# Performance work log

Hardware: AMD Instinct MI355X
Metric: run time of the kernel (lower is better)

## Reference

```python
import jax, jax.numpy as jnp
import numpy as np

N, D_IN, D_SAE, K = 8192, 768, 24576, 32


def setup_inputs() -> dict:
    key = jax.random.key(0)
    k1, k2, k3 = jax.random.split(key, 3)
    x = jax.random.normal(k1, (N, D_IN), dtype=jnp.float32)
    # kaiming_uniform_ on empty(d_in, d_sae): bound = sqrt(6 / d_in) (fan_in = d_sae? torch uses
    # fan_in = size(1) = d_sae for W_enc; we just need a same-scale random init for a reference)
    b_enc_bound = np.sqrt(6.0 / D_SAE)
    W_enc = jax.random.uniform(k2, (D_IN, D_SAE), dtype=jnp.float32,
                               minval=-b_enc_bound, maxval=b_enc_bound)
    b_dec_bound = np.sqrt(6.0 / D_IN)
    W_dec = jax.random.uniform(k3, (D_SAE, D_IN), dtype=jnp.float32,
                               minval=-b_dec_bound, maxval=b_dec_bound)
    # module normalizes decoder rows to unit L2 norm at init
    W_dec = W_dec / jnp.linalg.norm(W_dec, axis=1, keepdims=True)
    b_enc = jnp.zeros((D_SAE,), dtype=jnp.float32)
    b_dec = jnp.zeros((D_IN,), dtype=jnp.float32)
    return {"x": x, "W_enc": W_enc, "b_enc": b_enc, "W_dec": W_dec, "b_dec": b_dec}


def reference(x, W_enc, b_enc, W_dec, b_dec):
    # encode: relu((x - b_dec) @ W_enc + b_enc)
    z = jax.nn.relu((x - b_dec) @ W_enc + b_enc)            # [N, d_sae]
    topk_vals, topk_inds = jax.lax.top_k(z, K)              # [N, K]
    rows = jnp.arange(z.shape[0])[:, None]                  # [N, 1]
    z_sparse = jnp.zeros_like(z).at[rows, topk_inds].set(topk_vals)
    x_reconstruct = z_sparse @ W_dec + b_dec                # [N, d_in]
    return (x_reconstruct, z_sparse)
```

## Files before the change

kernel.cpp:

```cpp
#include <hip/hip_runtime.h>

#define N_ROWS 8192
#define D_IN   768
#define D_SAE  24576
#define K_TOP  32
#define C_SEL  40
#define DELTA  2e-4f

typedef __attribute__((ext_vector_type(8))) short bf16x8;
typedef __attribute__((ext_vector_type(4))) float f32x4;

__device__ __forceinline__ ushort f2bf(float f) {
    const unsigned u = __float_as_uint(f);
    return (ushort)((u + 0x7FFFu + ((u >> 16) & 1u)) >> 16);
}
__device__ __forceinline__ float bf2f(ushort h) {
    return __uint_as_float(((unsigned)h) << 16);
}

#define GBM 128
#define GBN 192
#define GBK 32

__global__ __launch_bounds__(256)
void sae_cvt_x(const float* __restrict__ x, const float* __restrict__ b_dec,
               ushort* __restrict__ ahi, ushort* __restrict__ alo)
{
    const int idx = blockIdx.x * 256 + threadIdx.x;
    const int i   = idx * 4;
    const int k   = (idx % (D_IN / 4)) * 4;
    const float4 xv = *(const float4*)(&x[i]);
    const float4 bd = *(const float4*)(&b_dec[k]);
    const float e[4] = {xv.x - bd.x, xv.y - bd.y, xv.z - bd.z, xv.w - bd.w};
    ushort h[4], l[4];
#pragma unroll
    for (int j = 0; j < 4; ++j) {
        h[j] = f2bf(e[j]);
        l[j] = f2bf(e[j] - bf2f(h[j]));
    }
    *(ushort4*)(&ahi[i]) = make_ushort4(h[0], h[1], h[2], h[3]);
    *(ushort4*)(&alo[i]) = make_ushort4(l[0], l[1], l[2], l[3]);
}

__global__ __launch_bounds__(256)
void sae_cvt_w(const float* __restrict__ W_enc,
               ushort* __restrict__ bhi, ushort* __restrict__ blo)
{
    __shared__ float tile[32][33];
    const int n0 = blockIdx.x * 32;
    const int k0 = blockIdx.y * 32;
    const int t  = threadIdx.x;
    const int r  = t >> 3;
    const int c4 = (t & 7) * 4;
    *(float4*)(&tile[r][c4]) = *(const float4*)(&W_enc[(size_t)(k0 + r) * D_SAE + n0 + c4]);
    __syncthreads();
    ushort h[4], l[4];
#pragma unroll
    for (int j = 0; j < 4; ++j) {
        const float e = tile[c4 + j][r];
        h[j] = f2bf(e);
        l[j] = f2bf(e - bf2f(h[j]));
    }
    *(ushort4*)(&bhi[(size_t)(n0 + r) * D_IN + k0 + c4]) = make_ushort4(h[0], h[1], h[2], h[3]);
    *(ushort4*)(&blo[(size_t)(n0 + r) * D_IN + k0 + c4]) = make_ushort4(l[0], l[1], l[2], l[3]);
}

__global__ __launch_bounds__(256, 2)
void sae_encode_mfma3(const ushort* __restrict__ ahi, const ushort* __restrict__ alo,
                      const ushort* __restrict__ bhi, const ushort* __restrict__ blo,
                      const float* __restrict__ b_enc, float* __restrict__ z)
{
    __shared__ ushort A_lds[2][2][4][GBM][8];
    __shared__ ushort B_lds[2][2][4][GBN][8];

    const int tid  = threadIdx.x;
    const int lane = tid & 63;
    const int wid  = tid >> 6;
    const int wr   = wid >> 1;
    const int wc   = wid & 1;
    const int l15  = lane & 15;
    const int lc   = lane >> 4;

    const int col0  = blockIdx.y * GBN;
    const int arow0 = blockIdx.x * GBM;
    const int row_w = arow0 + wr * 64;

    const int NT = D_IN / GBK;

    f32x4 acc[4][6];
#pragma unroll
    for (int i = 0; i < 4; ++i)
#pragma unroll
        for (int j = 0; j < 6; ++j) acc[i][j] = (f32x4){0.f, 0.f, 0.f, 0.f};

    bf16x8 s0, s1, s2, s3, s4, s5, s6, s7, s8, s9;

#define LOADQ(J, DST) { \
        const int q = (J) * 4 + wid; \
        if ((J) < 4) { \
            const int pl = q & 1, c = (q >> 1) & 3, h = q >> 3; \
            DST = *(const bf16x8*)((pl ? alo : ahi) + (size_t)(arow0 + h * 64 + lane) * D_IN + k0s + c * 8); \
        } else { \
            const int r2 = q - 16; \
            const int pl = r2 & 1, c = (r2 >> 1) & 3, g = r2 >> 3; \
            DST = *(const bf16x8*)((pl ? blo : bhi) + (size_t)(col0 + g * 64 + lane) * D_IN + k0s + c * 8); \
        } }

#define WRITEQ(J, SRC, BUF) { \
        const int q = (J) * 4 + wid; \
        if ((J) < 4) { \
            const int pl = q & 1, c = (q >> 1) & 3, h = q >> 3; \
            *(bf16x8*)(&A_lds[BUF][pl][c][h * 64 + lane][0]) = SRC; \
        } else { \
            const int r2 = q - 16; \
            const int pl = r2 & 1, c = (r2 >> 1) & 3, g = r2 >> 3; \
            *(bf16x8*)(&B_lds[BUF][pl][c][g * 64 + lane][0]) = SRC; \
        } }

#define LOAD_ALL() { LOADQ(0, s0) LOADQ(1, s1) LOADQ(2, s2) LOADQ(3, s3) LOADQ(4, s4) \
                     LOADQ(5, s5) LOADQ(6, s6) LOADQ(7, s7) LOADQ(8, s8) LOADQ(9, s9) }
#define WRITE_ALL(BUF) { WRITEQ(0, s0, BUF) WRITEQ(1, s1, BUF) WRITEQ(2, s2, BUF) WRITEQ(3, s3, BUF) \
                         WRITEQ(4, s4, BUF) WRITEQ(5, s5, BUF) WRITEQ(6, s6, BUF) WRITEQ(7, s7, BUF) \
                         WRITEQ(8, s8, BUF) WRITEQ(9, s9, BUF) }

    {
        const int k0s = 0;
        LOAD_ALL();
    }
    WRITE_ALL(0);
    __syncthreads();

    for (int kt = 0; kt < NT; ++kt) {
        const int cur = kt & 1;
        if (kt + 1 < NT) {
            const int k0s = (kt + 1) * GBK;
            LOAD_ALL();
        }

        bf16x8 bh[6], bl[6];
#pragma unroll
        for (int ct = 0; ct < 6; ++ct) {
            const int n = wc * 96 + ct * 16 + l15;
            bh[ct] = *(const bf16x8*)(&B_lds[cur][0][lc][n][0]);
            bl[ct] = *(const bf16x8*)(&B_lds[cur][1][lc][n][0]);
        }
#pragma unroll
        for (int rt = 0; rt < 4; ++rt) {
            const int m = wr * 64 + rt * 16 + l15;
            const bf16x8 ah = *(const bf16x8*)(&A_lds[cur][0][lc][m][0]);
            const bf16x8 al = *(const bf16x8*)(&A_lds[cur][1][lc][m][0]);
#pragma unroll
            for (int ct = 0; ct < 6; ++ct) {
                acc[rt][ct] = __builtin_amdgcn_mfma_f32_16x16x32_bf16(ah, bh[ct], acc[rt][ct], 0, 0, 0);
                acc[rt][ct] = __builtin_amdgcn_mfma_f32_16x16x32_bf16(ah, bl[ct], acc[rt][ct], 0, 0, 0);
                acc[rt][ct] = __builtin_amdgcn_mfma_f32_16x16x32_bf16(al, bh[ct], acc[rt][ct], 0, 0, 0);
            }
        }

        if (kt + 1 < NT) {
            WRITE_ALL(cur ^ 1);
            __syncthreads();
        }
    }

#undef LOAD_ALL
#undef WRITE_ALL
#undef LOADQ
#undef WRITEQ

#pragma unroll
    for (int ct = 0; ct < 6; ++ct) {
        const int col = col0 + wc * 96 + ct * 16 + l15;
        const float bec = b_enc[col];
#pragma unroll
        for (int rt = 0; rt < 4; ++rt) {
            const int rowb = row_w + rt * 16 + lc * 4;
#pragma unroll
            for (int r = 0; r < 4; ++r)
                z[(size_t)(rowb + r) * D_SAE + col] = fmaxf(acc[rt][ct][r] + bec, 0.f);
        }
    }
}

__global__ __launch_bounds__(256, 2)
void sae_encode_mfma(const float* __restrict__ x,
                     const float* __restrict__ W_enc,
                     const float* __restrict__ b_enc,
                     const float* __restrict__ b_dec,
                     float* __restrict__ z)
{
    __shared__ ushort Bs[2][4][GBN][8];

    const int tid  = threadIdx.x;
    const int lane = tid & 63;
    const int wid  = tid >> 6;
    const int wr   = wid >> 1;
    const int wc   = wid & 1;
    const int l15  = lane & 15;
    const int lc   = lane >> 4;

    const int col0  = blockIdx.x * GBN;
    const int row_w = blockIdx.y * GBM + wr * 64;

    f32x4 acc[4][6];
#pragma unroll
    for (int i = 0; i < 4; ++i)
#pragma unroll
        for (int j = 0; j < 6; ++j) acc[i][j] = (f32x4){0.f, 0.f, 0.f, 0.f};

    for (int kt = 0; kt < D_IN / GBK; ++kt) {
        const int k0 = kt * GBK;

        float bvv[3][8];
#pragma unroll
        for (int np = 0; np < 3; ++np)
#pragma unroll
            for (int it = 0; it < 8; ++it)
                bvv[np][it] = W_enc[(size_t)(k0 + wid * 8 + it) * D_SAE + col0 + np * 64 + lane];

        const float4 bd0 = *(const float4*)(&b_dec[k0 + lc * 8]);
        const float4 bd1 = *(const float4*)(&b_dec[k0 + lc * 8 + 4]);
        bf16x8 ah[4], al[4];
#pragma unroll
        for (int rt = 0; rt < 4; ++rt) {
            const size_t off = (size_t)(row_w + rt * 16 + l15) * D_IN + k0 + lc * 8;
            const float4 a0 = *(const float4*)(&x[off]);
            const float4 a1 = *(const float4*)(&x[off + 4]);
            float e[8];
            e[0] = a0.x - bd0.x; e[1] = a0.y - bd0.y; e[2] = a0.z - bd0.z; e[3] = a0.w - bd0.w;
            e[4] = a1.x - bd1.x; e[5] = a1.y - bd1.y; e[6] = a1.z - bd1.z; e[7] = a1.w - bd1.w;
#pragma unroll
            for (int j = 0; j < 8; ++j) {
                const ushort h = f2bf(e[j]);
                ah[rt][j] = (short)h;
                al[rt][j] = (short)f2bf(e[j] - bf2f(h));
            }
        }

        uint4 bh_pk[3], bl_pk[3];
#pragma unroll
        for (int np = 0; np < 3; ++np) {
            ushort h[8], l[8];
#pragma unroll
            for (int it = 0; it < 8; ++it) {
                h[it] = f2bf(bvv[np][it]);
                l[it] = f2bf(bvv[np][it] - bf2f(h[it]));
            }
            bh_pk[np] = make_uint4((unsigned)h[0] | ((unsigned)h[1] << 16),
                                   (unsigned)h[2] | ((unsigned)h[3] << 16),
                                   (unsigned)h[4] | ((unsigned)h[5] << 16),
                                   (unsigned)h[6] | ((unsigned)h[7] << 16));
            bl_pk[np] = make_uint4((unsigned)l[0] | ((unsigned)l[1] << 16),
                                   (unsigned)l[2] | ((unsigned)l[3] << 16),
                                   (unsigned)l[4] | ((unsigned)l[5] << 16),
                                   (unsigned)l[6] | ((unsigned)l[7] << 16));
        }

        __syncthreads();
#pragma unroll
        for (int np = 0; np < 3; ++np) {
            const int n = np * 64 + lane;
            *(uint4*)(&Bs[0][wid][n][0]) = bh_pk[np];
            *(uint4*)(&Bs[1][wid][n][0]) = bl_pk[np];
        }
        __syncthreads();

#pragma unroll
        for (int ct = 0; ct < 6; ++ct) {
            const int n = wc * 96 + ct * 16 + l15;
            const bf16x8 bh = *(const bf16x8*)(&Bs[0][lc][n][0]);
            const bf16x8 bl = *(const bf16x8*)(&Bs[1][lc][n][0]);
#pragma unroll
            for (int rt = 0; rt < 4; ++rt) {
                acc[rt][ct] = __builtin_amdgcn_mfma_f32_16x16x32_bf16(ah[rt], bh, acc[rt][ct], 0, 0, 0);
                acc[rt][ct] = __builtin_amdgcn_mfma_f32_16x16x32_bf16(ah[rt], bl, acc[rt][ct], 0, 0, 0);
                acc[rt][ct] = __builtin_amdgcn_mfma_f32_16x16x32_bf16(al[rt], bh, acc[rt][ct], 0, 0, 0);
            }
        }
    }

#pragma unroll
    for (int ct = 0; ct < 6; ++ct) {
        const int col = col0 + wc * 96 + ct * 16 + l15;
        const float bec = b_enc[col];
#pragma unroll
        for (int rt = 0; rt < 4; ++rt) {
            const int rowb = row_w + rt * 16 + lc * 4;
#pragma unroll
            for (int r = 0; r < 4; ++r)
                z[(size_t)(rowb + r) * D_SAE + col] = fmaxf(acc[rt][ct][r] + bec, 0.f);
        }
    }
}

#define TB     256
#define QPT    (D_SAE / 4 / TB)
#define HB     2048
#define NCOPY  2
#define BNDCAP 248
#define POOLN  288
#define NCAND  6
#define NEGF   -1e30f
#define BADIDX (1 << 30)

__global__ __launch_bounds__(TB, 4)
void sae_topk_decode(float* __restrict__ z,
                     const float* __restrict__ x,
                     const float* __restrict__ W_enc,
                     const float* __restrict__ b_enc,
                     const float* __restrict__ W_dec,
                     const float* __restrict__ b_dec,
                     float* __restrict__ x_rec)
{
    __shared__ int    hist[NCOPY * HB];
    __shared__ int    sufx[TB];
    __shared__ float  poolv[POOLN];
    __shared__ int    pooli[POOLN];
    __shared__ float  selv[C_SEL];
    __shared__ int    seli[C_SEL];
    __shared__ float  xrow[D_IN];
    __shared__ double cand[C_SEL];
    __shared__ int    shB, shChi;
    __shared__ int    nDef, nBnd, nFail;

    const int row = blockIdx.x;
    const int t   = threadIdx.x;
    const int w   = t >> 6;
    float* zr = z + (size_t)row * D_SAE;

    for (int i = t; i < NCOPY * HB; i += TB) hist[i] = 0;
    if (t == 0) { nDef = 0; nBnd = 0; nFail = 0; }
    __syncthreads();

    float cv[NCAND]; int ci[NCAND];
#pragma unroll
    for (int j = 0; j < NCAND; ++j) { cv[j] = NEGF; ci[j] = BADIDX; }
    {
        int* hw = &hist[(w >> 1) * HB];
        int zc = 0;
        for (int i0 = 0; i0 < QPT; i0 += 8) {
            f32x4 va[8];
#pragma unroll
            for (int u2 = 0; u2 < 8; ++u2)
                va[u2] = __builtin_nontemporal_load((const f32x4*)(&zr[(size_t)(t + (i0 + u2) * TB) * 4]));
#pragma unroll
            for (int u2 = 0; u2 < 8; ++u2) {
                const int base = (t + (i0 + u2) * TB) * 4;
#define PROC(f, o) { \
        const unsigned uu = __float_as_uint(f); \
        if (uu) atomicAdd(&hw[uu >> 20], 1); else ++zc; \
        const bool b0 = (f) > cv[0]; const bool b1 = (f) > cv[1]; const bool b2 = (f) > cv[2]; \
        const bool b3 = (f) > cv[3]; const bool b4 = (f) > cv[4]; const bool b5 = (f) > cv[5]; \
        if (b5) { \
            cv[5] = b4 ? cv[4] : (f);        ci[5] = b4 ? ci[4] : (base + o); \
            if (b4) { cv[4] = b3 ? cv[3] : (f); ci[4] = b3 ? ci[3] : (base + o); } \
            if (b3) { cv[3] = b2 ? cv[2] : (f); ci[3] = b2 ? ci[2] : (base + o); } \
            if (b2) { cv[2] = b1 ? cv[1] : (f); ci[2] = b1 ? ci[1] : (base + o); } \
            if (b1) { cv[1] = b0 ? cv[0] : (f); ci[1] = b0 ? ci[0] : (base + o); } \
            if (b0) { cv[0] = (f); ci[0] = (base + o); } \
        } }
                PROC(va[u2][0], 0) PROC(va[u2][1], 1) PROC(va[u2][2], 2) PROC(va[u2][3], 3)
#undef PROC
            }
        }
        if (zc) atomicAdd(&hw[0], zc);
    }
    __syncthreads();

    int cnt8[8]; int tot = 0;
#pragma unroll
    for (int j = 0; j < 8; ++j) {
        const int b = t * 8 + j;
        const int c = hist[b] + hist[HB + b];
        cnt8[j] = c; tot += c;
    }
    sufx[t] = tot;
    __syncthreads();
    for (int off = 1; off < TB; off <<= 1) {
        const int a = sufx[t];
        const int b = (t + off < TB) ? sufx[t + off] : 0;
        __syncthreads();
        sufx[t] = a + b;
        __syncthreads();
    }
    {
        int run = (t + 1 < TB) ? sufx[t + 1] : 0;
#pragma unroll
        for (int j = 7; j >= 0; --j) {
            const int c = cnt8[j];
            if (run < C_SEL && run + c >= C_SEL) { shB = t * 8 + j; shChi = run; }
            run += c;
        }
    }
    __syncthreads();
    const int B = shB;

    if (cv[NCAND - 1] > 0.f && (int)(__float_as_uint(cv[NCAND - 1]) >> 20) >= B) nFail = 1;
    __syncthreads();

    if (!nFail) {
#pragma unroll
        for (int j = 0; j < NCAND; ++j) {
            if (cv[j] > 0.f) {
                const int bk = (int)(__float_as_uint(cv[j]) >> 20);
                if (bk > B) {
                    const int p = atomicAdd(&nDef, 1);
                    poolv[p] = cv[j]; pooli[p] = ci[j];
                } else if (bk == B) {
                    const int p = atomicAdd(&nBnd, 1);
                    if (p < BNDCAP) { poolv[C_SEL + p] = cv[j]; pooli[C_SEL + p] = ci[j]; }
                }
            }
        }
    } else {
        for (int i = 0; i < QPT; ++i) {
            const float4 v = *(const float4*)(&zr[(size_t)(t + i * TB) * 4]);
            const int base = (t + i * TB) * 4;
#define COL(f, o) { const unsigned uu = __float_as_uint(f); if (uu) { const int bk = (int)(uu >> 20); \
            if (bk > B) { const int p = atomicAdd(&nDef, 1); poolv[p] = (f); pooli[p] = base + o; } \
            else if (bk == B) { const int p = atomicAdd(&nBnd, 1); if (p < BNDCAP) { poolv[C_SEL + p] = (f); pooli[C_SEL + p] = base + o; } } } }
            COL(v.x, 0) COL(v.y, 1) COL(v.z, 2) COL(v.w, 3)
#undef COL
        }
    }
    __syncthreads();

    {
        const int ndef  = nDef;
        const int nbndc = (nBnd < BNDCAP) ? nBnd : BNDCAP;
        for (int i = t; i < POOLN; i += TB)
            if (!(i < ndef) && !(i >= C_SEL && i < C_SEL + nbndc)) { poolv[i] = NEGF; pooli[i] = BADIDX; }
        if (t < C_SEL) { selv[t] = NEGF; seli[t] = BADIDX; }
    }
    __syncthreads();

    for (int e = t; e < POOLN; e += TB) {
        const float mv = poolv[e]; const int mi = pooli[e];
        int rank = 0;
        for (int j = 0; j < POOLN; ++j) {
            const float vj = poolv[j]; const int ij = pooli[j];
            if (vj > mv || (vj == mv && ij < mi)) ++rank;
        }
        if (rank < C_SEL && mi != BADIDX) { selv[rank] = mv; seli[rank] = mi; }
    }
    __syncthreads();

    if (selv[K_TOP - 1] - selv[K_TOP] < DELTA) {
        const int l = t & 63;
        for (int k = t; k < D_IN; k += TB) xrow[k] = x[(size_t)row * D_IN + k] - b_dec[k];
        __syncthreads();
        for (int j = w; j < C_SEL; j += 4) {
            const int c = seli[j];
            if (c < D_SAE) {
                double acc = 0.0;
#pragma unroll
                for (int q = 0; q < D_IN / 64; ++q) {
                    const int k = l + q * 64;
                    acc = fma((double)xrow[k], (double)W_enc[(size_t)k * D_SAE + c], acc);
                }
#pragma unroll
                for (int off = 32; off > 0; off >>= 1) acc += __shfl_down(acc, off);
                if (l == 0) {
                    const double vv = acc + (double)b_enc[c];
                    cand[j] = vv > 0.0 ? vv : 0.0;
                }
            } else if (l == 0) cand[j] = -1e300;
        }
        __syncthreads();
        if (t == 0) {
            bool used[C_SEL]; float nv[K_TOP]; int ni[K_TOP];
            for (int j = 0; j < C_SEL; ++j) used[j] = false;
            for (int s = 0; s < K_TOP; ++s) {
                int bj = -1; double bvv = 0.0; int bidx = 0;
                for (int j = 0; j < C_SEL; ++j) {
                    if (used[j]) continue;
                    const double v = cand[j]; const int idx = seli[j];
                    if (bj < 0 || v > bvv || (v == bvv && idx < bidx)) { bj = j; bvv = v; bidx = idx; }
                }
                used[bj] = true; nv[s] = (float)bvv; ni[s] = bidx;
            }
            for (int s = 0; s < K_TOP; ++s) { selv[s] = nv[s]; seli[s] = ni[s]; }
        }
        __syncthreads();
    }

    {
        const f32x4 z4 = (f32x4){0.f, 0.f, 0.f, 0.f};
        for (int i = 0; i < QPT; ++i)
            __builtin_nontemporal_store(z4, (f32x4*)(&zr[(size_t)(t + i * TB) * 4]));
    }
    __syncthreads();
    if (t < K_TOP && seli[t] < D_SAE) zr[seli[t]] = selv[t];

    float a0 = b_dec[t], a1 = b_dec[t + 256], a2 = b_dec[t + 512];
#pragma unroll 8
    for (int s = 0; s < K_TOP; ++s) {
        if (seli[s] < D_SAE) {
            const float v = selv[s];
            const float* wd = W_dec + (size_t)seli[s] * D_IN;
            a0 = fmaf(v, wd[t],       a0);
            a1 = fmaf(v, wd[t + 256], a1);
            a2 = fmaf(v, wd[t + 512], a2);
        }
    }
    float* xr = x_rec + (size_t)row * D_IN;
    xr[t] = a0; xr[t + 256] = a1; xr[t + 512] = a2;
}

extern "C" void kernel_launch(void* const* d_in, const int* in_sizes, int n_in,
                              void* d_out, int out_size, void* d_ws, size_t ws_size,
                              hipStream_t stream)
{
    const float* x     = (const float*)d_in[0];
    const float* W_enc = (const float*)d_in[1];
    const float* b_enc = (const float*)d_in[2];
    const float* W_dec = (const float*)d_in[3];
    const float* b_dec = (const float*)d_in[4];

    float* out   = (float*)d_out;
    float* x_rec = out;
    float* z     = out + (size_t)N_ROWS * D_IN;

    const size_t nA = (size_t)N_ROWS * D_IN;
    const size_t nB = (size_t)D_SAE * D_IN;
    const size_t need = (2 * nA + 2 * nB) * sizeof(ushort);

    if (ws_size >= need) {
        ushort* ahi = (ushort*)d_ws;
        ushort* alo = ahi + nA;
        ushort* bhi = alo + nA;
        ushort* blo = bhi + nB;
        sae_cvt_x<<<(int)(nA / 4 / 256), 256, 0, stream>>>(x, b_dec, ahi, alo);
        sae_cvt_w<<<dim3(D_SAE / 32, D_IN / 32), 256, 0, stream>>>(W_enc, bhi, blo);
        dim3 g1(N_ROWS / GBM, D_SAE / GBN);
        sae_encode_mfma3<<<g1, 256, 0, stream>>>(ahi, alo, bhi, blo, b_enc, z);
    } else {
        dim3 g0(D_SAE / GBN, N_ROWS / GBM);
        sae_encode_mfma<<<g0, 256, 0, stream>>>(x, W_enc, b_enc, b_dec, z);
    }
    sae_topk_decode<<<N_ROWS, TB, 0, stream>>>(z, x, W_enc, b_enc, W_dec, b_dec, x_rec);
}
```

Baseline: 2.120 ms.

## Use direct global-to-LDS loads, single-buffer LDS, raise occupancy in encoder GEMM

Replaces the register-staged double-buffered global→LDS copy in the split-bf16 encoder GEMM with global_load_lds direct-to-LDS transfers into a single LDS buffer. Launch bounds go from 2 to 4 waves per SIMD so more blocks can be resident and hide latency, relying on occupancy rather than in-block double buffering. In exchange, each k-step now waits for its loads to land before computing, with two barriers per iteration and no software prefetch. The occupancy bound may also force register spills, since the kernel holds 96 accumulator floats per thread.

```diff
diff --git a/kernel.cpp b/kernel.cpp
--- a/kernel.cpp
+++ b/kernel.cpp
@@ -65,13 +65,13 @@
     *(ushort4*)(&blo[(size_t)(n0 + r) * D_IN + k0 + c4]) = make_ushort4(l[0], l[1], l[2], l[3]);
 }
 
-__global__ __launch_bounds__(256, 2)
+__global__ __launch_bounds__(256, 4)
 void sae_encode_mfma3(const ushort* __restrict__ ahi, const ushort* __restrict__ alo,
                       const ushort* __restrict__ bhi, const ushort* __restrict__ blo,
                       const float* __restrict__ b_enc, float* __restrict__ z)
 {
-    __shared__ ushort A_lds[2][2][4][GBM][8];
-    __shared__ ushort B_lds[2][2][4][GBN][8];
+    __shared__ ushort A_lds[2][4][GBM][8];
+    __shared__ ushort B_lds[2][4][GBN][8];
 
     const int tid  = threadIdx.x;
     const int lane = tid & 63;
@@ -93,62 +93,39 @@
 #pragma unroll
         for (int j = 0; j < 6; ++j) acc[i][j] = (f32x4){0.f, 0.f, 0.f, 0.f};
 
-    bf16x8 s0, s1, s2, s3, s4, s5, s6, s7, s8, s9;
-
-#define LOADQ(J, DST) { \
+#define GLDSQ(J) { \
         const int q = (J) * 4 + wid; \
         if ((J) < 4) { \
             const int pl = q & 1, c = (q >> 1) & 3, h = q >> 3; \
-            DST = *(const bf16x8*)((pl ? alo : ahi) + (size_t)(arow0 + h * 64 + lane) * D_IN + k0s + c * 8); \
+            const ushort* gp = (pl ? alo : ahi) + (size_t)(arow0 + h * 64 + lane) * D_IN + k0s + c * 8; \
+            __builtin_amdgcn_global_load_lds((const __attribute__((address_space(1))) void*)gp, \
+                (__attribute__((address_space(3))) void*)&A_lds[pl][c][h * 64][0], 16, 0, 0); \
         } else { \
             const int r2 = q - 16; \
             const int pl = r2 & 1, c = (r2 >> 1) & 3, g = r2 >> 3; \
-            DST = *(const bf16x8*)((pl ? blo : bhi) + (size_t)(col0 + g * 64 + lane) * D_IN + k0s + c * 8); \
+            const ushort* gp = (pl ? blo : bhi) + (size_t)(col0 + g * 64 + lane) * D_IN + k0s + c * 8; \
+            __builtin_amdgcn_global_load_lds((const __attribute__((address_space(1))) void*)gp, \
+                (__attribute__((address_space(3))) void*)&B_lds[pl][c][g * 64][0], 16, 0, 0); \
         } }
 
-#define WRITEQ(J, SRC, BUF) { \
-        const int q = (J) * 4 + wid; \
-        if ((J) < 4) { \
-            const int pl = q & 1, c = (q >> 1) & 3, h = q >> 3; \
-            *(bf16x8*)(&A_lds[BUF][pl][c][h * 64 + lane][0]) = SRC; \
-        } else { \
-            const int r2 = q - 16; \
-            const int pl = r2 & 1, c = (r2 >> 1) & 3, g = r2 >> 3; \
-            *(bf16x8*)(&B_lds[BUF][pl][c][g * 64 + lane][0]) = SRC; \
-        } }
-
-#define LOAD_ALL() { LOADQ(0, s0) LOADQ(1, s1) LOADQ(2, s2) LOADQ(3, s3) LOADQ(4, s4) \
-                     LOADQ(5, s5) LOADQ(6, s6) LOADQ(7, s7) LOADQ(8, s8) LOADQ(9, s9) }
-#define WRITE_ALL(BUF) { WRITEQ(0, s0, BUF) WRITEQ(1, s1, BUF) WRITEQ(2, s2, BUF) WRITEQ(3, s3, BUF) \
-                         WRITEQ(4, s4, BUF) WRITEQ(5, s5, BUF) WRITEQ(6, s6, BUF) WRITEQ(7, s7, BUF) \
-                         WRITEQ(8, s8, BUF) WRITEQ(9, s9, BUF) }
-
-    {
-        const int k0s = 0;
-        LOAD_ALL();
-    }
-    WRITE_ALL(0);
-    __syncthreads();
-
     for (int kt = 0; kt < NT; ++kt) {
-        const int cur = kt & 1;
-        if (kt + 1 < NT) {
-            const int k0s = (kt + 1) * GBK;
-            LOAD_ALL();
-        }
+        const int k0s = kt * GBK;
+        GLDSQ(0) GLDSQ(1) GLDSQ(2) GLDSQ(3) GLDSQ(4)
+        GLDSQ(5) GLDSQ(6) GLDSQ(7) GLDSQ(8) GLDSQ(9)
+        __syncthreads();
 
         bf16x8 bh[6], bl[6];
 #pragma unroll
         for (int ct = 0; ct < 6; ++ct) {
             const int n = wc * 96 + ct * 16 + l15;
-            bh[ct] = *(const bf16x8*)(&B_lds[cur][0][lc][n][0]);
-            bl[ct] = *(const bf16x8*)(&B_lds[cur][1][lc][n][0]);
+            bh[ct] = *(const bf16x8*)(&B_lds[0][lc][n][0]);
+            bl[ct] = *(const bf16x8*)(&B_lds[1][lc][n][0]);
         }
 #pragma unroll
         for (int rt = 0; rt < 4; ++rt) {
             const int m = wr * 64 + rt * 16 + l15;
-            const bf16x8 ah = *(const bf16x8*)(&A_lds[cur][0][lc][m][0]);
-            const bf16x8 al = *(const bf16x8*)(&A_lds[cur][1][lc][m][0]);
+            const bf16x8 ah = *(const bf16x8*)(&A_lds[0][lc][m][0]);
+            const bf16x8 al = *(const bf16x8*)(&A_lds[1][lc][m][0]);
 #pragma unroll
             for (int ct = 0; ct < 6; ++ct) {
                 acc[rt][ct] = __builtin_amdgcn_mfma_f32_16x16x32_bf16(ah, bh[ct], acc[rt][ct], 0, 0, 0);
@@ -156,17 +133,9 @@
                 acc[rt][ct] = __builtin_amdgcn_mfma_f32_16x16x32_bf16(al, bh[ct], acc[rt][ct], 0, 0, 0);
             }
         }
-
-        if (kt + 1 < NT) {
-            WRITE_ALL(cur ^ 1);
-            __syncthreads();
-        }
-    }
-
-#undef LOAD_ALL
-#undef WRITE_ALL
-#undef LOADQ
-#undef WRITEQ
+        __syncthreads();
+    }
+#undef GLDSQ
 
 #pragma unroll
     for (int ct = 0; ct < 6; ++ct) {
```

New measurement: 5.946 ms. 181% more time.

## Deepen encoder GEMM prefetch to two K-tiles ahead with dual register sets

Applied to the files above, without the earlier changes.

Restructures the split-bf16 encoder GEMM main loop to hold two register staging sets (A and B) and unroll by two K-tiles. Global loads for a tile are now issued two iterations before they are written to LDS, which gives more latency hiding between load issue and use. The cost is doubled staging registers (20 bf16x8 vectors), which may pressure VGPRs and occupancy under the 256-thread launch bounds.

```diff
diff --git a/kernel.cpp b/kernel.cpp
--- a/kernel.cpp
+++ b/kernel.cpp
@@ -93,17 +93,18 @@
 #pragma unroll
         for (int j = 0; j < 6; ++j) acc[i][j] = (f32x4){0.f, 0.f, 0.f, 0.f};
 
-    bf16x8 s0, s1, s2, s3, s4, s5, s6, s7, s8, s9;
-
-#define LOADQ(J, DST) { \
+    bf16x8 sA0, sA1, sA2, sA3, sA4, sA5, sA6, sA7, sA8, sA9;
+    bf16x8 sB0, sB1, sB2, sB3, sB4, sB5, sB6, sB7, sB8, sB9;
+
+#define LOADQ(J, DST, K0S) { \
         const int q = (J) * 4 + wid; \
         if ((J) < 4) { \
             const int pl = q & 1, c = (q >> 1) & 3, h = q >> 3; \
-            DST = *(const bf16x8*)((pl ? alo : ahi) + (size_t)(arow0 + h * 64 + lane) * D_IN + k0s + c * 8); \
+            DST = *(const bf16x8*)((pl ? alo : ahi) + (size_t)(arow0 + h * 64 + lane) * D_IN + (K0S) + c * 8); \
         } else { \
             const int r2 = q - 16; \
             const int pl = r2 & 1, c = (r2 >> 1) & 3, g = r2 >> 3; \
-            DST = *(const bf16x8*)((pl ? blo : bhi) + (size_t)(col0 + g * 64 + lane) * D_IN + k0s + c * 8); \
+            DST = *(const bf16x8*)((pl ? blo : bhi) + (size_t)(col0 + g * 64 + lane) * D_IN + (K0S) + c * 8); \
         } }
 
 #define WRITEQ(J, SRC, BUF) { \
@@ -117,56 +118,60 @@
             *(bf16x8*)(&B_lds[BUF][pl][c][g * 64 + lane][0]) = SRC; \
         } }
 
-#define LOAD_ALL() { LOADQ(0, s0) LOADQ(1, s1) LOADQ(2, s2) LOADQ(3, s3) LOADQ(4, s4) \
-                     LOADQ(5, s5) LOADQ(6, s6) LOADQ(7, s7) LOADQ(8, s8) LOADQ(9, s9) }
-#define WRITE_ALL(BUF) { WRITEQ(0, s0, BUF) WRITEQ(1, s1, BUF) WRITEQ(2, s2, BUF) WRITEQ(3, s3, BUF) \
-                         WRITEQ(4, s4, BUF) WRITEQ(5, s5, BUF) WRITEQ(6, s6, BUF) WRITEQ(7, s7, BUF) \
-                         WRITEQ(8, s8, BUF) WRITEQ(9, s9, BUF) }
-
-    {
-        const int k0s = 0;
-        LOAD_ALL();
-    }
-    WRITE_ALL(0);
-    __syncthreads();
-
-    for (int kt = 0; kt < NT; ++kt) {
-        const int cur = kt & 1;
-        if (kt + 1 < NT) {
-            const int k0s = (kt + 1) * GBK;
-            LOAD_ALL();
-        }
-
-        bf16x8 bh[6], bl[6];
-#pragma unroll
-        for (int ct = 0; ct < 6; ++ct) {
-            const int n = wc * 96 + ct * 16 + l15;
-            bh[ct] = *(const bf16x8*)(&B_lds[cur][0][lc][n][0]);
-            bl[ct] = *(const bf16x8*)(&B_lds[cur][1][lc][n][0]);
-        }
-#pragma unroll
-        for (int rt = 0; rt < 4; ++rt) {
-            const int m = wr * 64 + rt * 16 + l15;
-            const bf16x8 ah = *(const bf16x8*)(&A_lds[cur][0][lc][m][0]);
-            const bf16x8 al = *(const bf16x8*)(&A_lds[cur][1][lc][m][0]);
-#pragma unroll
-            for (int ct = 0; ct < 6; ++ct) {
-                acc[rt][ct] = __builtin_amdgcn_mfma_f32_16x16x32_bf16(ah, bh[ct], acc[rt][ct], 0, 0, 0);
-                acc[rt][ct] = __builtin_amdgcn_mfma_f32_16x16x32_bf16(ah, bl[ct], acc[rt][ct], 0, 0, 0);
-                acc[rt][ct] = __builtin_amdgcn_mfma_f32_16x16x32_bf16(al, bh[ct], acc[rt][ct], 0, 0, 0);
-            }
-        }
-
-        if (kt + 1 < NT) {
-            WRITE_ALL(cur ^ 1);
-            __syncthreads();
-        }
-    }
-
-#undef LOAD_ALL
-#undef WRITE_ALL
+#define LOAD_SET_A(K0S) { LOADQ(0, sA0, K0S) LOADQ(1, sA1, K0S) LOADQ(2, sA2, K0S) LOADQ(3, sA3, K0S) LOADQ(4, sA4, K0S) \
+                          LOADQ(5, sA5, K0S) LOADQ(6, sA6, K0S) LOADQ(7, sA7, K0S) LOADQ(8, sA8, K0S) LOADQ(9, sA9, K0S) }
+#define LOAD_SET_B(K0S) { LOADQ(0, sB0, K0S) LOADQ(1, sB1, K0S) LOADQ(2, sB2, K0S) LOADQ(3, sB3, K0S) LOADQ(4, sB4, K0S) \
+                          LOADQ(5, sB5, K0S) LOADQ(6, sB6, K0S) LOADQ(7, sB7, K0S) LOADQ(8, sB8, K0S) LOADQ(9, sB9, K0S) }
+#define WRITE_SET_A(BUF) { WRITEQ(0, sA0, BUF) WRITEQ(1, sA1, BUF) WRITEQ(2, sA2, BUF) WRITEQ(3, sA3, BUF) WRITEQ(4, sA4, BUF) \
+                           WRITEQ(5, sA5, BUF) WRITEQ(6, sA6, BUF) WRITEQ(7, sA7, BUF) WRITEQ(8, sA8, BUF) WRITEQ(9, sA9, BUF) }
+#define WRITE_SET_B(BUF) { WRITEQ(0, sB0, BUF) WRITEQ(1, sB1, BUF) WRITEQ(2, sB2, BUF) WRITEQ(3, sB3, BUF) WRITEQ(4, sB4, BUF) \
+                           WRITEQ(5, sB5, BUF) WRITEQ(6, sB6, BUF) WRITEQ(7, sB7, BUF) WRITEQ(8, sB8, BUF) WRITEQ(9, sB9, BUF) }
+
+#define COMPUTE(BUF) { \
+        bf16x8 bh[6], bl[6]; \
+        _Pragma("unroll") \
+        for (int ct = 0; ct < 6; ++ct) { \
+            const int n = wc * 96 + ct * 16 + l15; \
+            bh[ct] = *(const bf16x8*)(&B_lds[BUF][0][lc][n][0]); \
+            bl[ct] = *(const bf16x8*)(&B_lds[BUF][1][lc][n][0]); \
+        } \
+        _Pragma("unroll") \
+        for (int rt = 0; rt < 4; ++rt) { \
+            const int m = wr * 64 + rt * 16 + l15; \
+            const bf16x8 ah = *(const bf16x8*)(&A_lds[BUF][0][lc][m][0]); \
+            const bf16x8 al = *(const bf16x8*)(&A_lds[BUF][1][lc][m][0]); \
+            _Pragma("unroll") \
+            for (int ct = 0; ct < 6; ++ct) { \
+                acc[rt][ct] = __builtin_amdgcn_mfma_f32_16x16x32_bf16(ah, bh[ct], acc[rt][ct], 0, 0, 0); \
+                acc[rt][ct] = __builtin_amdgcn_mfma_f32_16x16x32_bf16(ah, bl[ct], acc[rt][ct], 0, 0, 0); \
+                acc[rt][ct] = __builtin_amdgcn_mfma_f32_16x16x32_bf16(al, bh[ct], acc[rt][ct], 0, 0, 0); \
+            } \
+        } }
+
+    LOAD_SET_A(0)
+    WRITE_SET_A(0)
+    LOAD_SET_B(GBK)
+    __syncthreads();
+
+    for (int kt2 = 0; kt2 < NT; kt2 += 2) {
+        if (kt2 + 2 < NT) { LOAD_SET_A((kt2 + 2) * GBK) }
+        COMPUTE(0)
+        WRITE_SET_B(1)
+        __syncthreads();
+
+        if (kt2 + 3 < NT) { LOAD_SET_B((kt2 + 3) * GBK) }
+        COMPUTE(1)
+        if (kt2 + 2 < NT) { WRITE_SET_A(0) }
+        __syncthreads();
+    }
+
+#undef LOAD_SET_A
+#undef LOAD_SET_B
+#undef WRITE_SET_A
+#undef WRITE_SET_B
 #undef LOADQ
 #undef WRITEQ
+#undef COMPUTE
 
 #pragma unroll
     for (int ct = 0; ct < 6; ++ct) {
```

Measured after the change: 2.675 ms. 1.26x slower.
